# Kernel optimization log

Measured on AMD Instinct MI355X. Metric: run time of the kernel, lower is better.

The kernel has to match this reference:

```python
import jax, jax.numpy as jnp
import numpy as np
import math

MAX_SIZE = 2048  # max_size init arg


def setup_inputs() -> dict:
    key = jax.random.key(0)
    k1, k2, k3 = jax.random.split(key, 3)
    B, S, D = 16, 1024, 512
    PRED = 256
    data = jax.random.normal(k1, (B, S, D), dtype=jnp.float32)
    W = jax.random.normal(k2, (PRED, D), dtype=jnp.float32) * (1.0 / math.sqrt(D))
    b = jax.random.normal(k3, (PRED,), dtype=jnp.float32) * 0.01
    return {"data": data, "W": W, "b": b}


def reference(data, W, b):
    # data: [B, S, D]; self-attention with q=k=v=data
    B, S, D = data.shape
    pred_len = W.shape[0]
    scale = 1.0 / math.sqrt(D)
    scores = jnp.einsum('bsd,btd->bst', data, data) * scale          # [B,S,S]
    prob = jax.nn.softmax(scores, axis=-1)
    attn = jnp.einsum('bst,btd->bsd', prob, data)                     # [B,S,D]
    # NOTE: the original concatenates a 'mask' block (rows S..2S) onto attn,
    # but the per-timestep Linear loop only reads rows 0..S-1, so the mask
    # never affects the output (dead code). The loop collapses to one GEMM.
    lin = jnp.einsum('bsd,pd->bsp', attn, W) + b                      # [B,S,pred_len]
    out = jnp.zeros((B, MAX_SIZE, pred_len), dtype=data.dtype)
    out = out.at[:, :S, :].set(lin)
    return out
```

## Files before the change

### kernel.cpp

```cpp
#include <hip/hip_runtime.h>
#include <cstdint>
#include <cstddef>

#define B_    16
#define S_    1024
#define D_    512
#define P_    256
#define MAXS_ 2048

typedef unsigned short u16;
typedef unsigned int   u32;
typedef _Float16 f16;
typedef _Float16 f16x8 __attribute__((ext_vector_type(8)));
typedef float  f32x4  __attribute__((ext_vector_type(4)));
typedef unsigned short u16x4 __attribute__((ext_vector_type(4)));
typedef unsigned short u16x8 __attribute__((ext_vector_type(8)));

__device__ __forceinline__ void gld_lds16(const void* g, void* l) {
  __builtin_amdgcn_global_load_lds(
      (const __attribute__((address_space(1))) u32*)g,
      (__attribute__((address_space(3))) u32*)l, 16, 0, 0);
}

__device__ __forceinline__ u16 f2h(float f) {
  return __builtin_bit_cast(u16, (f16)f);
}
__device__ __forceinline__ float h2f(u16 h) {
  return (float)__builtin_bit_cast(f16, h);
}

template<int BPB>
__device__ __forceinline__ void xcd_map(int L, int& bz, int& r) {
  const int t = L & 7;
  const int j = L >> 3;
  bz = (t << 1) | (j / BPB);
  r  = j % BPB;
}

__global__ void convert_f16_kernel(const float* __restrict__ src, u16* __restrict__ dst, long n4) {
  long stride = (long)gridDim.x * blockDim.x;
  for (long i = (long)blockIdx.x * blockDim.x + threadIdx.x; i < n4; i += stride) {
    float4 v = ((const float4*)src)[i];
    u16x4 o;
    o[0] = f2h(v.x); o[1] = f2h(v.y); o[2] = f2h(v.z); o[3] = f2h(v.w);
    ((u16x4*)dst)[i] = o;
  }
}

__global__ __launch_bounds__(512, 2) void qk_pipe(
    const u16* __restrict__ A, u16* __restrict__ Cout, float scale) {
  extern __shared__ __align__(16) char smem[];
  const int tid  = threadIdx.x;
  const int lane = tid & 63;
  const int w    = tid >> 6;
  const int wm   = w >> 2;
  const int wn   = w & 3;
  const int lr   = lane & 15;
  const int hi   = lane >> 4;

  const int L = blockIdx.x + (blockIdx.y << 2) + (blockIdx.z << 4);
  int bz, r;
  xcd_map<16>(L, bz, r);
  const int I0 = (r >> 2) * 256;
  const int J0 = (r & 3) * 256;
  const u16* Ab = A + (long)bz * (S_ * D_);

  auto stageP = [&](int s, int part) {
    if (s >= 16) return;
    char* dst = smem + (s & 3) * 32768 + part * 16384;
    const int base = part ? J0 : I0;
    const int k0 = s * 32;
    #pragma unroll
    for (int i = 0; i < 2; ++i) {
      int cid   = i * 512 + tid;
      int inner = cid >> 2;
      int c     = (cid & 3) ^ ((inner >> 1) & 3);
      gld_lds16(Ab + (size_t)(base + inner) * D_ + k0 + c * 8, dst + cid * 16);
    }
  };

  f32x4 acc[8][4] = {};

  stageP(0, 0); stageP(0, 1);
  stageP(1, 0); stageP(1, 1);
  stageP(2, 0); stageP(2, 1);
  asm volatile("s_waitcnt vmcnt(8)" ::: "memory");
  __builtin_amdgcn_s_barrier();

  for (int s = 0; s < 16; ++s) {
    const char* sl = smem + (s & 3) * 32768;
    f16x8 bf[4];
    {
      f16x8 af[4];
      #pragma unroll
      for (int mq = 0; mq < 4; ++mq) {
        int row = wm * 128 + mq * 16 + lr;
        int cp  = hi ^ ((row >> 1) & 3);
        af[mq] = *(const f16x8*)(sl + row * 64 + cp * 16);
      }
      #pragma unroll
      for (int n = 0; n < 4; ++n) {
        int row = wn * 64 + n * 16 + lr;
        int cp  = hi ^ ((row >> 1) & 3);
        bf[n] = *(const f16x8*)(sl + 16384 + row * 64 + cp * 16);
      }
      stageP(s + 3, 0);
      __builtin_amdgcn_s_barrier();
      asm volatile("s_waitcnt lgkmcnt(0)" ::: "memory");
      __builtin_amdgcn_sched_barrier(0);
      __builtin_amdgcn_s_setprio(1);
      #pragma unroll
      for (int mq = 0; mq < 4; ++mq)
        #pragma unroll
        for (int n = 0; n < 4; ++n)
          acc[mq][n] = __builtin_amdgcn_mfma_f32_16x16x32_f16(af[mq], bf[n], acc[mq][n], 0, 0, 0);
      __builtin_amdgcn_s_setprio(0);
      __builtin_amdgcn_s_barrier();
    }
    {
      f16x8 af[4];
      #pragma unroll
      for (int mq = 0; mq < 4; ++mq) {
        int row = wm * 128 + 64 + mq * 16 + lr;
        int cp  = hi ^ ((row >> 1) & 3);
        af[mq] = *(const f16x8*)(sl + row * 64 + cp * 16);
      }
      stageP(s + 3, 1);
      __builtin_amdgcn_s_barrier();
      asm volatile("s_waitcnt lgkmcnt(0)" ::: "memory");
      __builtin_amdgcn_sched_barrier(0);
      __builtin_amdgcn_s_setprio(1);
      #pragma unroll
      for (int mq = 0; mq < 4; ++mq)
        #pragma unroll
        for (int n = 0; n < 4; ++n)
          acc[4 + mq][n] = __builtin_amdgcn_mfma_f32_16x16x32_f16(af[mq], bf[n], acc[4 + mq][n], 0, 0, 0);
      __builtin_amdgcn_s_setprio(0);
      if (s <= 12)      asm volatile("s_waitcnt vmcnt(8)" ::: "memory");
      else if (s == 13) asm volatile("s_waitcnt vmcnt(4)" ::: "memory");
      else if (s == 14) asm volatile("s_waitcnt vmcnt(0)" ::: "memory");
      __builtin_amdgcn_s_barrier();
    }
  }

  u16* Cb = Cout + (long)bz * S_ * S_;
  const int row0 = I0 + wm * 128;
  const int col0 = J0 + wn * 64;
  #pragma unroll
  for (int m = 0; m < 8; ++m) {
    #pragma unroll
    for (int i = 0; i < 4; ++i) {
      int rr = row0 + m * 16 + (hi << 2) + i;
      #pragma unroll
      for (int n = 0; n < 4; ++n) {
        int c = col0 + n * 16 + lr;
        Cb[(size_t)rr * S_ + c] = f2h(acc[m][n][i] * scale);
      }
    }
  }
}

__global__ __launch_bounds__(256) void stats_kernel(
    const u16* __restrict__ scores, float2* __restrict__ rowstat) {
  const int lane = threadIdx.x & 63;
  const int wv   = threadIdx.x >> 6;
  int bz, r;
  xcd_map<256>(blockIdx.x, bz, r);
  const long row = ((long)bz * 256 + r) * 4 + wv;
  const u16* src = scores + row * S_;

  u16x8 a0 = *(const u16x8*)&src[lane * 16];
  u16x8 a1 = *(const u16x8*)&src[lane * 16 + 8];
  float v[16];
  #pragma unroll
  for (int j = 0; j < 8; ++j) { v[j] = h2f(a0[j]); v[8 + j] = h2f(a1[j]); }

  float mx = v[0];
  #pragma unroll
  for (int j = 1; j < 16; ++j) mx = fmaxf(mx, v[j]);
  #pragma unroll
  for (int off = 32; off > 0; off >>= 1)
    mx = fmaxf(mx, __shfl_xor(mx, off));

  const float l2e = 1.4426950408889634f;
  float sum = 0.f;
  #pragma unroll
  for (int j = 0; j < 16; ++j) sum += exp2f((v[j] - mx) * l2e);
  #pragma unroll
  for (int off = 32; off > 0; off >>= 1)
    sum += __shfl_xor(sum, off);

  if (lane == 0) rowstat[row] = make_float2(mx, 1.f / sum);
}

__global__ __launch_bounds__(256, 2) void pv_slot(
    const u16* __restrict__ scores, const u16* __restrict__ VWT,
    const float2* __restrict__ rowstat,
    float* __restrict__ out, const float* __restrict__ bias) {
  extern __shared__ __align__(16) char smem[];
  const int tid  = threadIdx.x;
  const int lane = tid & 63;
  const int w    = tid >> 6;
  const int wm   = w >> 1;
  const int wn   = w & 1;
  const int lr   = lane & 15;
  const int hi   = lane >> 4;

  const int L = blockIdx.x + (blockIdx.y << 1) + (blockIdx.z << 6);
  int bz, rblk;
  xcd_map<64>(L, bz, rblk);
  const int yt = rblk >> 1;
  const int J0 = (rblk & 1) * 128;

  float* ob = out + (long)bz * MAXS_ * P_;
  if (yt >= 16) {
    #pragma unroll 2
    for (int i = tid; i < 64 * 32; i += 256) {
      int rr = i >> 5;
      int c4 = i & 31;
      *((float4*)(ob + (size_t)(yt * 64 + rr) * P_ + J0) + c4) =
          make_float4(0.f, 0.f, 0.f, 0.f);
    }
    return;
  }

  const int q0 = yt * 64;
  const u16* sA = scores + ((long)bz * S_ + q0) * S_;
  const u16* Vb = VWT + (long)bz * P_ * S_ + (size_t)J0 * S_;
  const float l2e = 1.4426950408889634f;

  const int ar0 = tid >> 3;
  const int ar1 = 32 + (tid >> 3);
  const int ac  = tid & 7;
  const int c0  = ac ^ (ar0 & 7);
  const int c1  = ac ^ (ar1 & 7);
  const float2 st0 = rowstat[(long)bz * S_ + q0 + ar0];
  const float2 st1 = rowstat[(long)bz * S_ + q0 + ar1];
  const float nml0 = -st0.x * l2e, il0 = st0.y;
  const float nml1 = -st1.x * l2e, il1 = st1.y;

  auto loadA = [&](int s, u16x8 (&r)[2]) {
    r[0] = *(const u16x8*)(sA + (size_t)ar0 * S_ + s * 64 + c0 * 8);
    r[1] = *(const u16x8*)(sA + (size_t)ar1 * S_ + s * 64 + c1 * 8);
  };
  auto writeA = [&](int buf, u16x8 (&r)[2]) {
    char* dA = smem + buf * 8192;
    u16x8 p0, p1;
    #pragma unroll
    for (int j = 0; j < 8; ++j) {
      p0[j] = f2h(exp2f(fmaf(h2f(r[0][j]), l2e, nml0)) * il0);
      p1[j] = f2h(exp2f(fmaf(h2f(r[1][j]), l2e, nml1)) * il1);
    }
    *(u16x8*)(dA + (size_t)tid * 16)         = p0;
    *(u16x8*)(dA + (size_t)(256 + tid) * 16) = p1;
  };
  auto stageB = [&](int s, int buf) {
    char* dB = smem + 24576 + buf * 16384;
    #pragma unroll
    for (int i = 0; i < 4; ++i) {
      int cid = i * 256 + tid;
      int row = cid >> 3;
      int c   = (cid & 7) ^ (row & 7);
      gld_lds16(Vb + (size_t)row * S_ + s * 64 + c * 8, dB + cid * 16);
    }
  };

  f32x4 acc[2][4] = {};
  u16x8 rA[2][2];

  loadA(0, rA[0]);
  __builtin_amdgcn_sched_barrier(0);
  stageB(0, 0);
  __builtin_amdgcn_sched_barrier(0);
  loadA(1, rA[1]);
  __builtin_amdgcn_sched_barrier(0);
  stageB(1, 1);
  __builtin_amdgcn_sched_barrier(0);
  asm volatile("s_waitcnt vmcnt(6)" ::: "memory");
  writeA(0, rA[0]);
  asm volatile("s_waitcnt lgkmcnt(0)" ::: "memory");
  __builtin_amdgcn_s_barrier();

  #pragma unroll
  for (int s = 0; s < 16; ++s) {
    const int bufR = s % 3;
    const char* aB = smem + bufR * 8192;
    const char* bB = smem + 24576 + bufR * 16384;

    f16x8 af[2][2], bf[2][4];
    #pragma unroll
    for (int kk = 0; kk < 2; ++kk) {
      #pragma unroll
      for (int m = 0; m < 2; ++m) {
        int row = wm * 32 + m * 16 + lr;
        int cp  = (kk * 4 + hi) ^ (row & 7);
        af[kk][m] = *(const f16x8*)(aB + row * 128 + cp * 16);
      }
      #pragma unroll
      for (int n = 0; n < 4; ++n) {
        int row = wn * 64 + n * 16 + lr;
        int cp  = (kk * 4 + hi) ^ (row & 7);
        bf[kk][n] = *(const f16x8*)(bB + row * 128 + cp * 16);
      }
    }

    if (s + 2 < 16) {
      loadA(s + 2, rA[s & 1]);
      __builtin_amdgcn_sched_barrier(0);
      stageB(s + 2, (s + 2) % 3);
      __builtin_amdgcn_sched_barrier(0);
    }

    __builtin_amdgcn_s_setprio(1);
    #pragma unroll
    for (int kk = 0; kk < 2; ++kk)
      #pragma unroll
      for (int m = 0; m < 2; ++m)
        #pragma unroll
        for (int n = 0; n < 4; ++n)
          acc[m][n] = __builtin_amdgcn_mfma_f32_16x16x32_f16(
              af[kk][m], bf[kk][n], acc[m][n], 0, 0, 0);
    __builtin_amdgcn_s_setprio(0);

    if (s < 15) {
      if (s <= 13) asm volatile("s_waitcnt vmcnt(6)" ::: "memory");
      else         asm volatile("s_waitcnt vmcnt(0)" ::: "memory");
      writeA((s + 1) % 3, rA[(s + 1) & 1]);
      asm volatile("s_waitcnt lgkmcnt(0)" ::: "memory");
      __builtin_amdgcn_s_barrier();
    }
  }

  float bv[4];
  #pragma unroll
  for (int n = 0; n < 4; ++n) bv[n] = bias[J0 + wn * 64 + n * 16 + lr];
  #pragma unroll
  for (int m = 0; m < 2; ++m) {
    #pragma unroll
    for (int i = 0; i < 4; ++i) {
      int rr = q0 + wm * 32 + m * 16 + (hi << 2) + i;
      #pragma unroll
      for (int n = 0; n < 4; ++n)
        ob[(size_t)rr * P_ + J0 + wn * 64 + n * 16 + lr] = acc[m][n][i] + bv[n];
    }
  }
}

template<int KK, int BM, int BN, int NW, int WNS, int BPB>
__global__ __launch_bounds__(NW * 64, 2) void gemm_nt_small(
    const u16* __restrict__ A, const u16* __restrict__ Bm,
    u16* __restrict__ C, long sAb, long sBb, long sCb, int LDC) {
  constexpr int T   = NW * 64;
  constexpr int WMS = NW / WNS;
  constexpr int MF  = BM / (WMS * 16);
  constexpr int NF  = BN / (WNS * 16);
  constexpr int LA  = BM * 8 / T;
  constexpr int LB  = BN * 8 / T;
  constexpr int SZ  = (BM + BN) * 128;
  constexpr int NT  = KK / 64;

  extern __shared__ __align__(16) char smem[];
  const int tid  = threadIdx.x;
  const int lane = tid & 63;
  const int w    = tid >> 6;
  const int wm   = w / WNS;
  const int wn   = w % WNS;
  const int lr   = lane & 15;
  const int hi   = lane >> 4;

  const int L = blockIdx.x + gridDim.x * (blockIdx.y + gridDim.y * blockIdx.z);
  int bz, r;
  xcd_map<BPB>(L, bz, r);
  const int I0 = (r / gridDim.x) * BM;
  const int J0 = (r % gridDim.x) * BN;
  const u16* Ab = A  + (long)bz * sAb;
  const u16* Bb = Bm + (long)bz * sBb;

  auto stage = [&](int buf, int k0) {
    char* sA = smem + buf * SZ;
    char* sB = sA + BM * 128;
    #pragma unroll
    for (int i = 0; i < LA; ++i) {
      int cid = i * T + tid;
      int row = cid >> 3;
      int c   = (cid & 7) ^ (row & 7);
      gld_lds16(Ab + (size_t)(I0 + row) * KK + k0 + c * 8, sA + cid * 16);
    }
    #pragma unroll
    for (int i = 0; i < LB; ++i) {
      int cid = i * T + tid;
      int row = cid >> 3;
      int c   = (cid & 7) ^ (row & 7);
      gld_lds16(Bb + (size_t)(J0 + row) * KK + k0 + c * 8, sB + cid * 16);
    }
  };

  f32x4 acc[MF][NF] = {};
  stage(0, 0);
  for (int t = 0; t < NT; ++t) {
    const char* lA = smem + (t & 1) * SZ;
    const char* lB = lA + BM * 128;
    if (t + 1 < NT) {
      stage((t + 1) & 1, (t + 1) * 64);
      asm volatile("s_waitcnt vmcnt(%0)" :: "i"(LA + LB) : "memory");
    } else {
      asm volatile("s_waitcnt vmcnt(0)" ::: "memory");
    }
    __builtin_amdgcn_s_barrier();
    __builtin_amdgcn_sched_barrier(0);
    #pragma unroll
    for (int kk = 0; kk < 2; ++kk) {
      f16x8 af[MF], bfv[NF];
      #pragma unroll
      for (int m = 0; m < MF; ++m) {
        int row = wm * (MF * 16) + m * 16 + lr;
        int cp  = (kk * 4 + hi) ^ (row & 7);
        af[m] = *(const f16x8*)(lA + ((row * 8 + cp) << 4));
      }
      #pragma unroll
      for (int n = 0; n < NF; ++n) {
        int row = wn * (NF * 16) + n * 16 + lr;
        int cp  = (kk * 4 + hi) ^ (row & 7);
        bfv[n] = *(const f16x8*)(lB + ((row * 8 + cp) << 4));
      }
      __builtin_amdgcn_s_setprio(1);
      #pragma unroll
      for (int m = 0; m < MF; ++m)
        #pragma unroll
        for (int n = 0; n < NF; ++n)
          acc[m][n] = __builtin_amdgcn_mfma_f32_16x16x32_f16(af[m], bfv[n], acc[m][n], 0, 0, 0);
      __builtin_amdgcn_s_setprio(0);
    }
    __builtin_amdgcn_sched_barrier(0);
    __builtin_amdgcn_s_barrier();
  }

  const int row0 = I0 + wm * (MF * 16);
  const int col0 = J0 + wn * (NF * 16);
  #pragma unroll
  for (int m = 0; m < MF; ++m)
    #pragma unroll
    for (int i = 0; i < 4; ++i) {
      int rr = row0 + m * 16 + (hi << 2) + i;
      #pragma unroll
      for (int n = 0; n < NF; ++n)
        C[(long)bz * sCb + (size_t)rr * LDC + col0 + n * 16 + lr] = f2h(acc[m][n][i]);
    }
}

extern "C" void kernel_launch(void* const* d_in, const int* in_sizes, int n_in,
                              void* d_out, int out_size, void* d_ws, size_t ws_size,
                              hipStream_t stream) {
  const float* data = (const float*)d_in[0];
  const float* W    = (const float*)d_in[1];
  const float* bias = (const float*)d_in[2];
  float* out = (float*)d_out;
  char*  ws  = (char*)d_ws;

  const size_t MB = 1024 * 1024;
  u16*    dataH   = (u16*)(ws);
  u16*    Wh      = (u16*)(ws + 16 * MB);
  u16*    scoresH = (u16*)(ws + 17 * MB);
  u16*    VWT     = (u16*)(ws + 49 * MB);
  float2* rowstat = (float2*)(ws + 57 * MB);

  const float scale = 0.04419417382415922f;

  constexpr int SMEM_QK = 4 * 32768;
  constexpr int SMEM_PV = 3 * 8192 + 3 * 16384;
  constexpr int SMEM_VW = 2 * (64 + 128) * 128;

  (void)hipFuncSetAttribute((const void*)&qk_pipe,
                      hipFuncAttributeMaxDynamicSharedMemorySize, SMEM_QK);
  (void)hipFuncSetAttribute((const void*)&pv_slot,
                      hipFuncAttributeMaxDynamicSharedMemorySize, SMEM_PV);
  (void)hipFuncSetAttribute((const void*)&gemm_nt_small<512, 64, 128, 4, 2, 32>,
                      hipFuncAttributeMaxDynamicSharedMemorySize, SMEM_VW);

  convert_f16_kernel<<<2048, 256, 0, stream>>>(data, dataH, (long)B_ * S_ * D_ / 4);
  convert_f16_kernel<<<64, 256, 0, stream>>>(W, Wh, (long)P_ * D_ / 4);

  gemm_nt_small<512, 64, 128, 4, 2, 32><<<dim3(8, 4, 16), 256, SMEM_VW, stream>>>(
      Wh, dataH, VWT, 0L, (long)S_ * D_, (long)P_ * S_, S_);

  qk_pipe<<<dim3(4, 4, 16), 512, SMEM_QK, stream>>>(dataH, scoresH, scale);

  stats_kernel<<<4096, 256, 0, stream>>>(scoresH, rowstat);

  pv_slot<<<dim3(2, 32, 16), 256, SMEM_PV, stream>>>(
      scoresH, VWT, rowstat, out, bias);
}
```

Baseline: 78.41 us.

## Fuse softmax row statistics into QK epilogue and use nontemporal stores

Removes the separate stats kernel. The QK GEMM epilogue now computes per-tile row max and sum-exp with shuffles and an LDS merge, then writes partial stats for each of the four column tiles, and the PV kernel merges them. This avoids re-reading the 32MB fp16 score matrix and one kernel launch. It also switches score stores, output stores and score loads to nontemporal hints, at the cost of extra epilogue work and a sync in QK.

After: 83.38 us. 6.3% more time.

```diff
diff --git a/kernel.cpp b/kernel.cpp
--- a/kernel.cpp
+++ b/kernel.cpp
@@ -48,7 +48,8 @@
 }
 
 __global__ __launch_bounds__(512, 2) void qk_pipe(
-    const u16* __restrict__ A, u16* __restrict__ Cout, float scale) {
+    const u16* __restrict__ A, u16* __restrict__ Cout,
+    float2* __restrict__ rowpart, float scale) {
   extern __shared__ __align__(16) char smem[];
   const int tid  = threadIdx.x;
   const int lane = tid & 63;
@@ -143,6 +144,9 @@
     }
   }
 
+  __syncthreads();
+  float2* part = (float2*)smem;
+  const float l2e = 1.4426950408889634f;
   u16* Cb = Cout + (long)bz * S_ * S_;
   const int row0 = I0 + wm * 128;
   const int col0 = J0 + wn * 64;
@@ -151,51 +155,41 @@
     #pragma unroll
     for (int i = 0; i < 4; ++i) {
       int rr = row0 + m * 16 + (hi << 2) + i;
-      #pragma unroll
-      for (int n = 0; n < 4; ++n) {
-        int c = col0 + n * 16 + lr;
-        Cb[(size_t)rr * S_ + c] = f2h(acc[m][n][i] * scale);
-      }
-    }
-  }
-}
-
-__global__ __launch_bounds__(256) void stats_kernel(
-    const u16* __restrict__ scores, float2* __restrict__ rowstat) {
-  const int lane = threadIdx.x & 63;
-  const int wv   = threadIdx.x >> 6;
-  int bz, r;
-  xcd_map<256>(blockIdx.x, bz, r);
-  const long row = ((long)bz * 256 + r) * 4 + wv;
-  const u16* src = scores + row * S_;
-
-  u16x8 a0 = *(const u16x8*)&src[lane * 16];
-  u16x8 a1 = *(const u16x8*)&src[lane * 16 + 8];
-  float v[16];
-  #pragma unroll
-  for (int j = 0; j < 8; ++j) { v[j] = h2f(a0[j]); v[8 + j] = h2f(a1[j]); }
-
-  float mx = v[0];
-  #pragma unroll
-  for (int j = 1; j < 16; ++j) mx = fmaxf(mx, v[j]);
-  #pragma unroll
-  for (int off = 32; off > 0; off >>= 1)
-    mx = fmaxf(mx, __shfl_xor(mx, off));
-
-  const float l2e = 1.4426950408889634f;
-  float sum = 0.f;
-  #pragma unroll
-  for (int j = 0; j < 16; ++j) sum += exp2f((v[j] - mx) * l2e);
-  #pragma unroll
-  for (int off = 32; off > 0; off >>= 1)
-    sum += __shfl_xor(sum, off);
-
-  if (lane == 0) rowstat[row] = make_float2(mx, 1.f / sum);
+      float v[4];
+      #pragma unroll
+      for (int n = 0; n < 4; ++n) v[n] = acc[m][n][i] * scale;
+      float mx = fmaxf(fmaxf(v[0], v[1]), fmaxf(v[2], v[3]));
+      #pragma unroll
+      for (int off = 1; off <= 8; off <<= 1)
+        mx = fmaxf(mx, __shfl_xor(mx, off));
+      float sum = 0.f;
+      #pragma unroll
+      for (int n = 0; n < 4; ++n) sum += exp2f((v[n] - mx) * l2e);
+      #pragma unroll
+      for (int off = 1; off <= 8; off <<= 1)
+        sum += __shfl_xor(sum, off);
+      #pragma unroll
+      for (int n = 0; n < 4; ++n)
+        __builtin_nontemporal_store(f2h(v[n]),
+            &Cb[(size_t)rr * S_ + col0 + n * 16 + lr]);
+      if (lr == 0)
+        part[(wm * 128 + m * 16 + (hi << 2) + i) * 4 + wn] = make_float2(mx, sum);
+    }
+  }
+  __syncthreads();
+  if (tid < 256) {
+    float2 a = part[tid * 4],     b = part[tid * 4 + 1];
+    float2 c = part[tid * 4 + 2], d = part[tid * 4 + 3];
+    float m = fmaxf(fmaxf(a.x, b.x), fmaxf(c.x, d.x));
+    float l = a.y * exp2f((a.x - m) * l2e) + b.y * exp2f((b.x - m) * l2e)
+            + c.y * exp2f((c.x - m) * l2e) + d.y * exp2f((d.x - m) * l2e);
+    rowpart[((long)bz * 4 + (J0 >> 8)) * S_ + I0 + tid] = make_float2(m, l);
+  }
 }
 
 __global__ __launch_bounds__(256, 2) void pv_slot(
     const u16* __restrict__ scores, const u16* __restrict__ VWT,
-    const float2* __restrict__ rowstat,
+    const float2* __restrict__ rowpart,
     float* __restrict__ out, const float* __restrict__ bias) {
   extern __shared__ __align__(16) char smem[];
   const int tid  = threadIdx.x;
@@ -214,12 +208,13 @@
 
   float* ob = out + (long)bz * MAXS_ * P_;
   if (yt >= 16) {
+    f32x4 z = {0.f, 0.f, 0.f, 0.f};
     #pragma unroll 2
     for (int i = tid; i < 64 * 32; i += 256) {
       int rr = i >> 5;
       int c4 = i & 31;
-      *((float4*)(ob + (size_t)(yt * 64 + rr) * P_ + J0) + c4) =
-          make_float4(0.f, 0.f, 0.f, 0.f);
+      __builtin_nontemporal_store(z,
+          (f32x4*)(ob + (size_t)(yt * 64 + rr) * P_ + J0) + c4);
     }
     return;
   }
@@ -234,14 +229,26 @@
   const int ac  = tid & 7;
   const int c0  = ac ^ (ar0 & 7);
   const int c1  = ac ^ (ar1 & 7);
-  const float2 st0 = rowstat[(long)bz * S_ + q0 + ar0];
-  const float2 st1 = rowstat[(long)bz * S_ + q0 + ar1];
-  const float nml0 = -st0.x * l2e, il0 = st0.y;
-  const float nml1 = -st1.x * l2e, il1 = st1.y;
+
+  const float2* rp = rowpart + (long)bz * 4 * S_;
+  auto mergeStat = [&](int row, float& nml, float& il) {
+    float2 a = rp[row],          b = rp[S_ + row];
+    float2 c = rp[2 * S_ + row], d = rp[3 * S_ + row];
+    float m = fmaxf(fmaxf(a.x, b.x), fmaxf(c.x, d.x));
+    float l = a.y * exp2f((a.x - m) * l2e) + b.y * exp2f((b.x - m) * l2e)
+            + c.y * exp2f((c.x - m) * l2e) + d.y * exp2f((d.x - m) * l2e);
+    nml = -m * l2e;
+    il  = 1.f / l;
+  };
+  float nml0, il0, nml1, il1;
+  mergeStat(q0 + ar0, nml0, il0);
+  mergeStat(q0 + ar1, nml1, il1);
 
   auto loadA = [&](int s, u16x8 (&r)[2]) {
-    r[0] = *(const u16x8*)(sA + (size_t)ar0 * S_ + s * 64 + c0 * 8);
-    r[1] = *(const u16x8*)(sA + (size_t)ar1 * S_ + s * 64 + c1 * 8);
+    r[0] = __builtin_nontemporal_load(
+        (const u16x8*)(sA + (size_t)ar0 * S_ + s * 64 + c0 * 8));
+    r[1] = __builtin_nontemporal_load(
+        (const u16x8*)(sA + (size_t)ar1 * S_ + s * 64 + c1 * 8));
   };
   auto writeA = [&](int buf, u16x8 (&r)[2]) {
     char* dA = smem + buf * 8192;
@@ -341,7 +348,8 @@
       int rr = q0 + wm * 32 + m * 16 + (hi << 2) + i;
       #pragma unroll
       for (int n = 0; n < 4; ++n)
-        ob[(size_t)rr * P_ + J0 + wn * 64 + n * 16 + lr] = acc[m][n][i] + bv[n];
+        __builtin_nontemporal_store(acc[m][n][i] + bv[n],
+            &ob[(size_t)rr * P_ + J0 + wn * 64 + n * 16 + lr]);
     }
   }
 }
@@ -462,7 +470,7 @@
   u16*    Wh      = (u16*)(ws + 16 * MB);
   u16*    scoresH = (u16*)(ws + 17 * MB);
   u16*    VWT     = (u16*)(ws + 49 * MB);
-  float2* rowstat = (float2*)(ws + 57 * MB);
+  float2* rowpart = (float2*)(ws + 57 * MB);
 
   const float scale = 0.04419417382415922f;
 
@@ -483,10 +491,9 @@
   gemm_nt_small<512, 64, 128, 4, 2, 32><<<dim3(8, 4, 16), 256, SMEM_VW, stream>>>(
       Wh, dataH, VWT, 0L, (long)S_ * D_, (long)P_ * S_, S_);
 
-  qk_pipe<<<dim3(4, 4, 16), 512, SMEM_QK, stream>>>(dataH, scoresH, scale);
-
-  stats_kernel<<<4096, 256, 0, stream>>>(scoresH, rowstat);
+  qk_pipe<<<dim3(4, 4, 16), 512, SMEM_QK, stream>>>(
+      dataH, scoresH, rowpart, scale);
 
   pv_slot<<<dim3(2, 32, 16), 256, SMEM_PV, stream>>>(
-      scoresH, VWT, rowstat, out, bias);
-}
+      scoresH, VWT, rowpart, out, bias);
+}
```
